# Performance work log

Measured on AMD Instinct MI355X. Metric: run time of the kernel, lower is better.

## Reference

```python
import jax, jax.numpy as jnp
import numpy as np

B_DIM, C_DIM, K_DIM, L_DIM = 16, 64, 207, 64
SUPPORT_LEN, ORDER = 2, 2
C_IN = (ORDER * SUPPORT_LEN + 1) * C_DIM  # 320, include_self=True


def setup_inputs() -> dict:
    key = jax.random.key(0)
    k1, k2, k3, k4 = jax.random.split(key, 4)
    x = jax.random.normal(k1, (B_DIM, C_DIM, K_DIM * L_DIM), dtype=jnp.float32)
    # per-batch adaptive adjacencies (B, K, K), nonnegative like softmax(relu(E1 E2^T))
    a0 = jax.random.uniform(k2, (B_DIM, K_DIM, K_DIM), dtype=jnp.float32)
    a1 = jax.random.uniform(k3, (B_DIM, K_DIM, K_DIM), dtype=jnp.float32)
    # 1x1 conv weight (C_out, C_in) and bias
    W = jax.random.normal(k4, (C_DIM, C_IN), dtype=jnp.float32) * (1.0 / np.sqrt(C_IN))
    b = jnp.zeros((C_DIM,), dtype=jnp.float32)
    return {"x": x, "a0": a0, "a1": a1, "W": W, "b": b, "K": K_DIM, "L": L_DIM}


def reference(x, a0, a1, W, b, K, L):
    B, C = x.shape[0], x.shape[1]
    x = x.reshape(B, C, K, L)  # (B, C, K, L)
    # torch: x1[bl, c, j] = sum_k x[bl, c, k] * a[b, j, k]  (bmm with a^T)
    diffuse = lambda h, a: jnp.einsum('bckl,bjk->bcjl', h, a)
    out = [x]  # include_self=True
    for a in (a0, a1):
        x1 = diffuse(x, a)
        out.append(x1)
        for _ in range(2, ORDER + 1):
            x1 = diffuse(x1, a)
            out.append(x1)
    h = jnp.concatenate(out, axis=1)  # (B, 5C, K, L)
    y = jnp.einsum('bikl,oi->bokl', h, W) + b[None, :, None, None]  # 1x1 conv
    return y.reshape(B, C, K * L)
```

## Files before the change

kernel.cpp:

```cpp
#include <hip/hip_runtime.h>

typedef unsigned short u16;
typedef __bf16 bf16x8 __attribute__((ext_vector_type(8)));
typedef float f32x4 __attribute__((ext_vector_type(4)));

#define NB 16
#define NC 64
#define NK 207
#define NL 64
#define KP 224
#define NKL 13248
#define CIN 320


__device__ __forceinline__ u16 f2bf(float f) {
  unsigned u = __builtin_bit_cast(unsigned, f);
  u += 0x7FFFu + ((u >> 16) & 1u);
  return (u16)(u >> 16);
}

__device__ __forceinline__ void g2l16(const u16* gsrc, u16* ldst) {
  __builtin_amdgcn_global_load_lds(
      (const __attribute__((address_space(1))) unsigned int*)gsrc,
      (__attribute__((address_space(3))) unsigned int*)ldst, 16, 0, 0);
}

__global__ __launch_bounds__(256) void k_prepx(
    const float* __restrict__ x, const float* __restrict__ W,
    u16* __restrict__ Xf, u16* __restrict__ Wbf) {
  __shared__ __align__(16) u16 xs[16 * 2048];
  int id = blockIdx.x, t = threadIdx.x;
  if (id < 512) {
    int b = id >> 5, rem = id & 31;
    int c4 = rem >> 3, lh = (rem >> 1) & 3, ksh = rem & 1;
    int ks0 = ksh ? 4 : 0, nks = ksh ? 3 : 4;
    int kw = nks * 32;
    int l0 = lh * 16;
    int cl = t >> 4, kl = t & 15;
    const float* xc = x + (size_t)(b * 64 + c4 * 16 + cl) * NKL;
    for (int kk = kl; kk < kw; kk += 16) {
      int k = ksh * 128 + kk;
      float4 v0 = {0.f, 0.f, 0.f, 0.f}, v1 = v0, v2 = v0, v3 = v0;
      if (k < NK) {
        const float4* p = (const float4*)(xc + (size_t)k * 64 + l0);
        v0 = p[0]; v1 = p[1]; v2 = p[2]; v3 = p[3];
      }
      int ksl = kk >> 5, q = (kk >> 3) & 3, e = kk & 7;
      u16* dst = &xs[ksl * 512 + (cl + 16 * q) * 8 + e];
      dst[0 * 2048] = f2bf(v0.x);  dst[1 * 2048] = f2bf(v0.y);
      dst[2 * 2048] = f2bf(v0.z);  dst[3 * 2048] = f2bf(v0.w);
      dst[4 * 2048] = f2bf(v1.x);  dst[5 * 2048] = f2bf(v1.y);
      dst[6 * 2048] = f2bf(v1.z);  dst[7 * 2048] = f2bf(v1.w);
      dst[8 * 2048] = f2bf(v2.x);  dst[9 * 2048] = f2bf(v2.y);
      dst[10 * 2048] = f2bf(v2.z); dst[11 * 2048] = f2bf(v2.w);
      dst[12 * 2048] = f2bf(v3.x); dst[13 * 2048] = f2bf(v3.y);
      dst[14 * 2048] = f2bf(v3.z); dst[15 * 2048] = f2bf(v3.w);
    }
    __syncthreads();
    int wavei = t >> 6, lane = t & 63;
    u16* Xb = Xf + (size_t)b * 256 * 7 * 512;
    for (int ll = wavei; ll < 16; ll += 4) {
      int l = l0 + ll;
      for (int ksl = 0; ksl < nks; ksl++) {
        bf16x8 v = *(const bf16x8*)&xs[ll * 2048 + ksl * 512 + lane * 8];
        *(bf16x8*)(Xb + ((size_t)(l * 4 + c4) * 7 + ks0 + ksl) * 512 +
                   lane * 8) = v;
      }
    }
  } else {
    for (int ci = t; ci < 2560; ci += 256) {
      int o = ci / 40, kc = ci - o * 40;
      u16 v[8] __attribute__((aligned(16)));
      for (int j = 0; j < 8; j++) v[j] = f2bf(W[o * CIN + kc * 8 + j]);
      *(int4*)(Wbf + ((size_t)(o >> 4) * 10 + (kc >> 2)) * 512 +
               ((o & 15) + 16 * (kc & 3)) * 8) = *(int4*)v;
    }
  }
}

#define ACOL 50176
__global__ __launch_bounds__(512) void k_prepa(
    const float* __restrict__ a0, const float* __restrict__ a1,
    u16* __restrict__ Gf) {
  __shared__ __align__(16) u16 al[64512];
  int bw = blockIdx.x;
  int b = bw >> 1, w = bw & 1;
  int t = threadIdx.x;
  int wave = t >> 6, lane = t & 63;
  int r = lane & 15, q = lane >> 4;
  const float* A = (w ? a1 : a0) + (size_t)b * NK * NK;

  for (int u = t; u < 6272; u += 512) {
    int m = u / 28, kc = u - m * 28;
    u16 v[8] __attribute__((aligned(16)));
#pragma unroll
    for (int j = 0; j < 8; j++) {
      int k = kc * 8 + j;
      v[j] = (m < NK && k < NK) ? f2bf(A[(size_t)m * NK + k]) : (u16)0;
    }
    *(int4*)&al[((m >> 4) * 7 + (kc >> 2)) * 512 +
                ((m & 15) + 16 * (kc & 3)) * 8] = *(int4*)v;
  }
  __syncthreads();

  u16* Gp13 = Gf + ((size_t)b * 5 + 1 + 2 * w) * 13 * 7 * 512;
  for (int f = wave; f < 91; f += 8) {
    bf16x8 v = *(const bf16x8*)&al[(size_t)f * 512 + lane * 8];
    *(bf16x8*)(Gp13 + (size_t)f * 512 + lane * 8) = v;
  }

  if (w == 0) {
    u16* Gp0 = Gf + (size_t)b * 5 * 13 * 7 * 512;
    for (int u = t; u < 91 * 64; u += 512) {
      int f = u >> 6, pos = u & 63;
      int jt = f / 7, ks = f - jt * 7;
      int j = jt * 16 + (pos & 15), qq = pos >> 4;
      u16 v[8] __attribute__((aligned(16)));
#pragma unroll
      for (int e = 0; e < 8; e++) {
        int k = ks * 32 + qq * 8 + e;
        v[e] = (j == k && j < NK) ? (u16)0x3F80 : (u16)0;
      }
      *(int4*)(Gp0 + (size_t)f * 512 + pos * 8) = *(int4*)v;
    }
  }

  u16* Gp24 = Gf + ((size_t)b * 5 + 2 + 2 * w) * 13 * 7 * 512;
  for (int ch = 0; ch < 4; ch++) {
    int n0 = ch * 64;
    __syncthreads();
    {
      int n = n0 + lane;
      for (int mi = 0; mi < 28; mi++) {
        int m = wave * 28 + mi;
        u16 v = (n < NK && m < NK) ? f2bf(A[(size_t)m * NK + n]) : (u16)0;
        al[ACOL + ((lane >> 4) * 7 + (m >> 5)) * 512 +
           ((lane & 15) + 16 * ((m >> 3) & 3)) * 8 + (m & 7)] = v;
      }
    }
    __syncthreads();
    for (int o = wave; o < 56; o += 8) {
      int mt = o >> 2, nt = o & 3;
      f32x4 acc = {};
#pragma unroll
      for (int ks = 0; ks < 7; ks++) {
        bf16x8 af = *(const bf16x8*)&al[(mt * 7 + ks) * 512 + lane * 8];
        bf16x8 bg = *(const bf16x8*)&al[ACOL + (nt * 7 + ks) * 512 + lane * 8];
        acc = __builtin_amdgcn_mfma_f32_16x16x32_bf16(af, bg, acc, 0, 0, 0);
      }
#pragma unroll
      for (int rr = 0; rr < 4; rr++) {
        int mj = mt * 16 + q * 4 + rr;
        int nk = n0 + nt * 16 + r;
        if (mj < 208 && nk < KP)
          Gp24[((size_t)(mj >> 4) * 7 + (nk >> 5)) * 512 +
               ((mj & 15) + 16 * ((nk >> 3) & 3)) * 8 + (nk & 7)] =
              f2bf(acc[rr]);
      }
    }
  }
}

#define AG 17920
__global__ __launch_bounds__(512, 4) void k_fused(
    const u16* __restrict__ Gf, const u16* __restrict__ Xf,
    const u16* __restrict__ Wbf, const float* __restrict__ bias,
    float* __restrict__ y) {
  __shared__ __align__(16) u16 lds[AG + 2 * 8192];
  int id = blockIdx.x;
  int wg = (id & 7) * 416 + (id >> 3);
  int b = wg / 208, rem = wg % 208;
  int jt = rem >> 4, lt = rem & 15;
  int tid = threadIdx.x, wave = tid >> 6, lane = tid & 63;
  int r = lane & 15, q = lane >> 4;
  const u16* Gb = Gf + (size_t)b * 5 * 13 * 7 * 512;
  const u16* Xw = Xf + ((size_t)b * 256 + lt * 16) * 7 * 512;

  for (int i2 = 0; i2 < 5; i2++) {
    int tile = i2 * 8 + wave;
    if (tile < 35) {
      int p = tile / 7, ks = tile - p * 7;
      g2l16(Gb + ((size_t)(p * 13 + jt) * 7 + ks) * 512 + lane * 8,
            &lds[tile * 512 + lane * 8]);
    }
  }
  for (int i2 = 0; i2 < 2; i2++) {
    int tl = wave * 2 + i2;
    g2l16(Xw + (size_t)tl * 7 * 512 + lane * 8, &lds[AG + tl * 512 + lane * 8]);
  }
  asm volatile("s_waitcnt vmcnt(2)" ::: "memory");
  __builtin_amdgcn_s_barrier();

  f32x4 acc1[5][2] = {};
#pragma unroll
  for (int ks = 0; ks < 7; ks++) {
    int cur = ks & 1;
    if (ks < 6) {
      for (int i2 = 0; i2 < 2; i2++) {
        int tl = wave * 2 + i2;
        g2l16(Xw + ((size_t)tl * 7 + ks + 1) * 512 + lane * 8,
              &lds[AG + (cur ^ 1) * 8192 + tl * 512 + lane * 8]);
      }
      asm volatile("s_waitcnt vmcnt(2)" ::: "memory");
    } else {
      asm volatile("s_waitcnt vmcnt(0)" ::: "memory");
    }
    bf16x8 af0 = *(const bf16x8*)&lds[AG + cur * 8192 + (wave * 2 + 0) * 512 + lane * 8];
    bf16x8 af1 = *(const bf16x8*)&lds[AG + cur * 8192 + (wave * 2 + 1) * 512 + lane * 8];
    __builtin_amdgcn_s_setprio(1);
#pragma unroll
    for (int p = 0; p < 5; p++) {
      bf16x8 bg = *(const bf16x8*)&lds[(p * 7 + ks) * 512 + lane * 8];
      acc1[p][0] = __builtin_amdgcn_mfma_f32_16x16x32_bf16(af0, bg, acc1[p][0], 0, 0, 0);
      acc1[p][1] = __builtin_amdgcn_mfma_f32_16x16x32_bf16(af1, bg, acc1[p][1], 0, 0, 0);
    }
    __builtin_amdgcn_s_setprio(0);
  }
  __syncthreads();

#pragma unroll
  for (int p = 0; p < 5; p++)
#pragma unroll
    for (int mf = 0; mf < 2; mf++) {
      int m = (wave * 2 + mf) * 16 + q * 4;
      int tt = m >> 6, c = m & 63;
      int cs = c ^ ((r & 7) << 3);
      int idxT = ((p * 16 + r) * 4 + tt) * 72 + cs;
      u16 v0 = f2bf(acc1[p][mf][0]), v1 = f2bf(acc1[p][mf][1]);
      u16 v2 = f2bf(acc1[p][mf][2]), v3 = f2bf(acc1[p][mf][3]);
      *(uint2*)&lds[idxT] = make_uint2((unsigned)v0 | ((unsigned)v1 << 16),
                                       (unsigned)v2 | ((unsigned)v3 << 16));
    }
  int mo = wave >> 1, nh = (wave & 1) * 2;
  const u16* Wt = Wbf + (size_t)mo * 10 * 512 + lane * 8;
  bf16x8 aw[10];
#pragma unroll
  for (int ks = 0; ks < 10; ks++) aw[ks] = *(const bf16x8*)(Wt + ks * 512);
  __syncthreads();

  f32x4 acc2[2] = {};
#pragma unroll
  for (int ks = 0; ks < 10; ks++) {
    int p = ks >> 1, c0 = (ks & 1) * 32;
#pragma unroll
    for (int nf = 0; nf < 2; nf++) {
      int n = (nh + nf) * 16 + r;
      int j = n >> 2, tt = n & 3;
      int cs = (c0 + q * 8) ^ ((j & 7) << 3);
      bf16x8 bt = *(const bf16x8*)&lds[((p * 16 + j) * 4 + tt) * 72 + cs];
      acc2[nf] = __builtin_amdgcn_mfma_f32_16x16x32_bf16(aw[ks], bt, acc2[nf], 0, 0, 0);
    }
  }

  int o0 = mo * 16 + q * 4;
  float4 bv = *(const float4*)&bias[o0];
  float* yb = y + (size_t)b * 64 * NKL;
#pragma unroll
  for (int nf = 0; nf < 2; nf++) {
    int n = (nh + nf) * 16 + r;
    int j = n >> 2, tt = n & 3;
    int jnode = jt * 16 + j;
    if (jnode < NK) {
      int col = jnode * 64 + lt * 4 + tt;
      yb[(size_t)(o0 + 0) * NKL + col] = acc2[nf][0] + bv.x;
      yb[(size_t)(o0 + 1) * NKL + col] = acc2[nf][1] + bv.y;
      yb[(size_t)(o0 + 2) * NKL + col] = acc2[nf][2] + bv.z;
      yb[(size_t)(o0 + 3) * NKL + col] = acc2[nf][3] + bv.w;
    }
  }
}

extern "C" void kernel_launch(void* const* d_in, const int* in_sizes, int n_in,
                              void* d_out, int out_size, void* d_ws, size_t ws_size,
                              hipStream_t stream) {
  const float* x = (const float*)d_in[0];
  const float* a0 = (const float*)d_in[1];
  const float* a1 = (const float*)d_in[2];
  const float* W = (const float*)d_in[3];
  const float* bias = (const float*)d_in[4];
  float* y = (float*)d_out;
  char* ws = (char*)d_ws;

  size_t off = 0;
  auto alloc = [&](size_t bytes) {
    size_t o = off;
    off = (off + bytes + 511) & ~(size_t)511;
    return o;
  };
  size_t o_Xf = alloc((size_t)NB * 256 * 7 * 512 * 2);
  size_t o_Gf = alloc((size_t)NB * 5 * 13 * 7 * 512 * 2);
  size_t o_Wf = alloc((size_t)4 * 10 * 512 * 2);
  (void)ws_size;

  u16* Xf = (u16*)(ws + o_Xf);
  u16* Gf = (u16*)(ws + o_Gf);
  u16* Wf = (u16*)(ws + o_Wf);

  k_prepa<<<dim3(32), 512, 0, stream>>>(a0, a1, Gf);
  k_prepx<<<dim3(513), 256, 0, stream>>>(x, W, Xf, Wf);
  k_fused<<<dim3(16 * 13 * 16), 512, 0, stream>>>(Gf, Xf, Wf, bias, y);
}
```

Baseline: 222.1 us.

## Merge adjacency and x prep into one kernel with finer A² tiling

```diff
diff --git a/kernel.cpp b/kernel.cpp
--- a/kernel.cpp
+++ b/kernel.cpp
@@ -25,10 +25,11 @@
       (__attribute__((address_space(3))) unsigned int*)ldst, 16, 0, 0);
 }
 
-__global__ __launch_bounds__(256) void k_prepx(
-    const float* __restrict__ x, const float* __restrict__ W,
-    u16* __restrict__ Xf, u16* __restrict__ Wbf) {
-  __shared__ __align__(16) u16 xs[16 * 2048];
+__global__ __launch_bounds__(256) void k_prep(
+    const float* __restrict__ x, const float* __restrict__ a0,
+    const float* __restrict__ a1, const float* __restrict__ W,
+    u16* __restrict__ Xf, u16* __restrict__ Gf, u16* __restrict__ Wbf) {
+  __shared__ __align__(16) u16 sm[32768];
   int id = blockIdx.x, t = threadIdx.x;
   if (id < 512) {
     int b = id >> 5, rem = id & 31;
@@ -46,7 +47,7 @@
         v0 = p[0]; v1 = p[1]; v2 = p[2]; v3 = p[3];
       }
       int ksl = kk >> 5, q = (kk >> 3) & 3, e = kk & 7;
-      u16* dst = &xs[ksl * 512 + (cl + 16 * q) * 8 + e];
+      u16* dst = &sm[ksl * 512 + (cl + 16 * q) * 8 + e];
       dst[0 * 2048] = f2bf(v0.x);  dst[1 * 2048] = f2bf(v0.y);
       dst[2 * 2048] = f2bf(v0.z);  dst[3 * 2048] = f2bf(v0.w);
       dst[4 * 2048] = f2bf(v1.x);  dst[5 * 2048] = f2bf(v1.y);
@@ -62,10 +63,92 @@
     for (int ll = wavei; ll < 16; ll += 4) {
       int l = l0 + ll;
       for (int ksl = 0; ksl < nks; ksl++) {
-        bf16x8 v = *(const bf16x8*)&xs[ll * 2048 + ksl * 512 + lane * 8];
+        bf16x8 v = *(const bf16x8*)&sm[ll * 2048 + ksl * 512 + lane * 8];
         *(bf16x8*)(Xb + ((size_t)(l * 4 + c4) * 7 + ks0 + ksl) * 512 +
                    lane * 8) = v;
       }
+    }
+  } else if (id < 1024) {
+    int local = id - 512;
+    int bw = local >> 4, tp = local & 15;
+    int b = bw >> 1, w = bw & 1;
+    int m0 = (tp >> 2) * 64, n0 = (tp & 3) * 64;
+    const float* A = (w ? a1 : a0) + (size_t)b * NK * NK;
+    for (int u = t; u < 64 * 28; u += 256) {
+      int ml = u / 28, kc = u - ml * 28;
+      int m = m0 + ml;
+      u16 v[8] __attribute__((aligned(16)));
+#pragma unroll
+      for (int j = 0; j < 8; j++) {
+        int k = kc * 8 + j;
+        v[j] = (m < NK && k < NK) ? f2bf(A[(size_t)m * NK + k]) : (u16)0;
+      }
+      *(int4*)&sm[((ml >> 4) * 7 + (kc >> 2)) * 512 +
+                  ((ml & 15) + 16 * (kc & 3)) * 8] = *(int4*)v;
+    }
+    {
+      int nl = t & 63, mq = t >> 6;
+      int n = n0 + nl;
+      for (int mi = 0; mi < 56; mi++) {
+        int m = mq * 56 + mi;
+        u16 v = (n < NK && m < NK) ? f2bf(A[(size_t)m * NK + n]) : (u16)0;
+        sm[14336 + ((nl >> 4) * 7 + (m >> 5)) * 512 +
+           ((nl & 15) + 16 * ((m >> 3) & 3)) * 8 + (m & 7)] = v;
+      }
+    }
+    __syncthreads();
+    int lane = t & 63, wave = t >> 6;
+    int r = lane & 15, q = lane >> 4;
+    u16* Gp24 = Gf + ((size_t)b * 5 + 2 + 2 * w) * 13 * 7 * 512;
+    for (int o = wave; o < 16; o += 4) {
+      int mf = o >> 2, nf = o & 3;
+      f32x4 acc = {};
+#pragma unroll
+      for (int ks = 0; ks < 7; ks++) {
+        bf16x8 af = *(const bf16x8*)&sm[(mf * 7 + ks) * 512 + lane * 8];
+        bf16x8 bg = *(const bf16x8*)&sm[14336 + (nf * 7 + ks) * 512 + lane * 8];
+        acc = __builtin_amdgcn_mfma_f32_16x16x32_bf16(af, bg, acc, 0, 0, 0);
+      }
+#pragma unroll
+      for (int rr = 0; rr < 4; rr++) {
+        int mj = m0 + mf * 16 + q * 4 + rr;
+        int nk = n0 + nf * 16 + r;
+        if (mj < 208 && nk < KP)
+          Gp24[((size_t)(mj >> 4) * 7 + (nk >> 5)) * 512 +
+               ((mj & 15) + 16 * ((nk >> 3) & 3)) * 8 + (nk & 7)] =
+              f2bf(acc[rr]);
+      }
+    }
+  } else if (id < 1280) {
+    int local = id - 1024;
+    int rt = local & 7, bw = local >> 3;
+    int b = bw >> 1, w = bw & 1;
+    const float* A = (w ? a1 : a0) + (size_t)b * NK * NK;
+    u16* Gp13 = Gf + ((size_t)b * 5 + 1 + 2 * w) * 13 * 7 * 512;
+    int m0 = rt * 26;
+    for (int u = t; u < 26 * 28; u += 256) {
+      int ml = u / 28, kc = u - ml * 28;
+      int m = m0 + ml;
+      u16 v[8] __attribute__((aligned(16)));
+#pragma unroll
+      for (int j = 0; j < 8; j++) {
+        int k = kc * 8 + j;
+        v[j] = (m < NK && k < NK) ? f2bf(A[(size_t)m * NK + k]) : (u16)0;
+      }
+      *(int4*)(Gp13 + ((size_t)(m >> 4) * 7 + (kc >> 2)) * 512 +
+               ((m & 15) + 16 * (kc & 3)) * 8) = *(int4*)v;
+    }
+  } else if (id < 1312) {
+    int local = id - 1280, b = local >> 1, half = local & 1;
+    u16* Gp0 = Gf + (size_t)b * 5 * 13 * 7 * 512;
+    for (int ci = t; ci < 104 * 28; ci += 256) {
+      int jr = ci / 28, kc = ci - jr * 28;
+      int j = half * 104 + jr;
+      u16 v[8] __attribute__((aligned(16)));
+      for (int jj = 0; jj < 8; jj++)
+        v[jj] = (j == kc * 8 + jj && j < NK) ? (u16)0x3F80 : (u16)0;
+      *(int4*)(Gp0 + ((size_t)(j >> 4) * 7 + (kc >> 2)) * 512 +
+               ((j & 15) + 16 * (kc & 3)) * 8) = *(int4*)v;
     }
   } else {
     for (int ci = t; ci < 2560; ci += 256) {
@@ -74,89 +157,6 @@
       for (int j = 0; j < 8; j++) v[j] = f2bf(W[o * CIN + kc * 8 + j]);
       *(int4*)(Wbf + ((size_t)(o >> 4) * 10 + (kc >> 2)) * 512 +
                ((o & 15) + 16 * (kc & 3)) * 8) = *(int4*)v;
-    }
-  }
-}
-
-#define ACOL 50176
-__global__ __launch_bounds__(512) void k_prepa(
-    const float* __restrict__ a0, const float* __restrict__ a1,
-    u16* __restrict__ Gf) {
-  __shared__ __align__(16) u16 al[64512];
-  int bw = blockIdx.x;
-  int b = bw >> 1, w = bw & 1;
-  int t = threadIdx.x;
-  int wave = t >> 6, lane = t & 63;
-  int r = lane & 15, q = lane >> 4;
-  const float* A = (w ? a1 : a0) + (size_t)b * NK * NK;
-
-  for (int u = t; u < 6272; u += 512) {
-    int m = u / 28, kc = u - m * 28;
-    u16 v[8] __attribute__((aligned(16)));
-#pragma unroll
-    for (int j = 0; j < 8; j++) {
-      int k = kc * 8 + j;
-      v[j] = (m < NK && k < NK) ? f2bf(A[(size_t)m * NK + k]) : (u16)0;
-    }
-    *(int4*)&al[((m >> 4) * 7 + (kc >> 2)) * 512 +
-                ((m & 15) + 16 * (kc & 3)) * 8] = *(int4*)v;
-  }
-  __syncthreads();
-
-  u16* Gp13 = Gf + ((size_t)b * 5 + 1 + 2 * w) * 13 * 7 * 512;
-  for (int f = wave; f < 91; f += 8) {
-    bf16x8 v = *(const bf16x8*)&al[(size_t)f * 512 + lane * 8];
-    *(bf16x8*)(Gp13 + (size_t)f * 512 + lane * 8) = v;
-  }
-
-  if (w == 0) {
-    u16* Gp0 = Gf + (size_t)b * 5 * 13 * 7 * 512;
-    for (int u = t; u < 91 * 64; u += 512) {
-      int f = u >> 6, pos = u & 63;
-      int jt = f / 7, ks = f - jt * 7;
-      int j = jt * 16 + (pos & 15), qq = pos >> 4;
-      u16 v[8] __attribute__((aligned(16)));
-#pragma unroll
-      for (int e = 0; e < 8; e++) {
-        int k = ks * 32 + qq * 8 + e;
-        v[e] = (j == k && j < NK) ? (u16)0x3F80 : (u16)0;
-      }
-      *(int4*)(Gp0 + (size_t)f * 512 + pos * 8) = *(int4*)v;
-    }
-  }
-
-  u16* Gp24 = Gf + ((size_t)b * 5 + 2 + 2 * w) * 13 * 7 * 512;
-  for (int ch = 0; ch < 4; ch++) {
-    int n0 = ch * 64;
-    __syncthreads();
-    {
-      int n = n0 + lane;
-      for (int mi = 0; mi < 28; mi++) {
-        int m = wave * 28 + mi;
-        u16 v = (n < NK && m < NK) ? f2bf(A[(size_t)m * NK + n]) : (u16)0;
-        al[ACOL + ((lane >> 4) * 7 + (m >> 5)) * 512 +
-           ((lane & 15) + 16 * ((m >> 3) & 3)) * 8 + (m & 7)] = v;
-      }
-    }
-    __syncthreads();
-    for (int o = wave; o < 56; o += 8) {
-      int mt = o >> 2, nt = o & 3;
-      f32x4 acc = {};
-#pragma unroll
-      for (int ks = 0; ks < 7; ks++) {
-        bf16x8 af = *(const bf16x8*)&al[(mt * 7 + ks) * 512 + lane * 8];
-        bf16x8 bg = *(const bf16x8*)&al[ACOL + (nt * 7 + ks) * 512 + lane * 8];
-        acc = __builtin_amdgcn_mfma_f32_16x16x32_bf16(af, bg, acc, 0, 0, 0);
-      }
-#pragma unroll
-      for (int rr = 0; rr < 4; rr++) {
-        int mj = mt * 16 + q * 4 + rr;
-        int nk = n0 + nt * 16 + r;
-        if (mj < 208 && nk < KP)
-          Gp24[((size_t)(mj >> 4) * 7 + (nk >> 5)) * 512 +
-               ((mj & 15) + 16 * ((nk >> 3) & 3)) * 8 + (nk & 7)] =
-              f2bf(acc[rr]);
-      }
     }
   }
 }
@@ -296,7 +296,6 @@
   u16* Gf = (u16*)(ws + o_Gf);
   u16* Wf = (u16*)(ws + o_Wf);
 
-  k_prepa<<<dim3(32), 512, 0, stream>>>(a0, a1, Gf);
-  k_prepx<<<dim3(513), 256, 0, stream>>>(x, W, Xf, Wf);
+  k_prep<<<dim3(1313), 256, 0, stream>>>(x, a0, a1, W, Xf, Gf, Wf);
   k_fused<<<dim3(16 * 13 * 16), 512, 0, stream>>>(Gf, Xf, Wf, bias, y);
 }
```

Measured after the change: 208.9 us. 5.9% less time.
